# Optimization experiments

Hardware: AMD Instinct MI355X
Metric: run time of the kernel (lower is better)

The kernel has to match this reference:

```python
import jax, jax.numpy as jnp
import numpy as np

N_QUBITS = 4
DIM = 2 ** N_QUBITS  # 16-dim statevector
KERNEL = 3
STRIDE = 1
PADDING = 1


def _rot_mats(w):
    # PennyLane Rot(phi, theta, omega) = RZ(omega) RY(theta) RZ(phi)
    phi, theta, omega = w[:, 0], w[:, 1], w[:, 2]
    c = jnp.cos(theta / 2)
    s = jnp.sin(theta / 2)
    em = jnp.exp(-0.5j * (phi + omega))
    ep = jnp.exp(0.5j * (phi + omega))
    ed = jnp.exp(0.5j * (phi - omega))
    edm = jnp.exp(-0.5j * (phi - omega))
    row0 = jnp.stack([em * c, -ed * s], axis=-1)
    row1 = jnp.stack([edm * s, ep * c], axis=-1)
    return jnp.stack([row0, row1], axis=-2)  # [n_qubits, 2, 2]


def _apply_1q(state, U, wire):
    # state: [M] + [2]*n, wire axis is 1+wire (wire 0 is most significant)
    s = jnp.moveaxis(state, 1 + wire, -1)
    s = jnp.einsum('...b,ab->...a', s, U)
    return jnp.moveaxis(s, -1, 1 + wire)


def _apply_cnot(state, c, t):
    s = jnp.moveaxis(state, (1 + c, 1 + t), (-2, -1))
    shp = s.shape
    s = s.reshape(shp[:-2] + (4,))[..., jnp.array([0, 1, 3, 2])].reshape(shp)
    return jnp.moveaxis(s, (-2, -1), (1 + c, 1 + t))


def _forward(x, W_pre, b_pre, W_post, b_post, q_weights):
    B, C, L = x.shape
    xp = jnp.pad(x, ((0, 0), (0, 0), (PADDING, PADDING)))
    L_out = (L + 2 * PADDING - KERNEL) // STRIDE + 1
    starts = jnp.arange(L_out) * STRIDE
    # windows: [B, C, L_out, K] -> flatten channel-major like torch reshape
    win = xp[:, :, starts[:, None] + jnp.arange(KERNEL)[None, :]]
    win = win.transpose(0, 2, 1, 3).reshape(B, L_out, C * KERNEL)
    pre = win @ W_pre.T + b_pre  # [B, L_out, n_qubits]
    # AmplitudeEmbedding: pad to 2**n and normalize
    v = jnp.pad(pre, ((0, 0), (0, 0), (0, DIM - N_QUBITS)))
    v = v / jnp.linalg.norm(v, axis=-1, keepdims=True)
    state = v.reshape(B * L_out, *([2] * N_QUBITS)).astype(jnp.complex64)
    U = _rot_mats(q_weights)
    for i in range(N_QUBITS):
        state = _apply_1q(state, U[i], i)
    for i in range(N_QUBITS - 1):
        state = _apply_cnot(state, i, i + 1)
    flat = state.reshape(B * L_out, DIM)
    probs = jnp.real(flat) ** 2 + jnp.imag(flat) ** 2
    # PauliZ expectation per wire: sign of bit i (wire 0 = MSB)
    bits = (jnp.arange(DIM)[None, :] >> (N_QUBITS - 1 - jnp.arange(N_QUBITS)[:, None])) & 1
    z = (1 - 2 * bits).astype(probs.dtype)  # [n_qubits, DIM]
    expz = (probs @ z.T).reshape(B, L_out, N_QUBITS)
    out = expz @ W_post.T + b_post  # [B, L_out, out_channels]
    return out.transpose(0, 2, 1)


def setup_inputs() -> dict:
    key = jax.random.key(0)
    ks = jax.random.split(key, 6)
    B, C, L = 32, 80, 3000
    OUT = 512
    return {
        'x': jax.random.normal(ks[0], (B, C, L), dtype=jnp.float32),
        'W_pre': jax.random.normal(ks[1], (N_QUBITS, C * KERNEL), dtype=jnp.float32) * 0.06,
        'b_pre': jax.random.normal(ks[2], (N_QUBITS,), dtype=jnp.float32) * 0.06,
        'W_post': jax.random.normal(ks[3], (OUT, N_QUBITS), dtype=jnp.float32) * 0.4,
        'b_post': jax.random.normal(ks[4], (OUT,), dtype=jnp.float32) * 0.4,
        'q_weights': jax.random.normal(ks[5], (N_QUBITS, 3), dtype=jnp.float32),
    }


def reference(x, W_pre, b_pre, W_post, b_post, q_weights):
    return _forward(x, W_pre, b_pre, W_post, b_post, q_weights)
```

## Files before the change

### kernel.cpp

```cpp
#include <hip/hip_runtime.h>
#include <math.h>

#define C_IN 80
#define L_IN 3000
#define OUT_C 512
#define NT 256
#define TL 128

struct c2f { float x, y; };

__device__ __forceinline__ c2f cmul(c2f a, c2f b) {
    return { a.x*b.x - a.y*b.y, a.x*b.y + a.y*b.x };
}
__device__ __forceinline__ c2f csel(c2f a, c2f b, int bit) {
    c2f r; r.x = bit ? b.x : a.x; r.y = bit ? b.y : a.y; return r;
}
__device__ __forceinline__ float quadform(const float4* __restrict__ A, float4 p) {
    float4 r0 = A[0], r1 = A[1], r2 = A[2], r3 = A[3];
    return p.x*(r0.x*p.x + r0.y*p.y + r0.z*p.z + r0.w*p.w)
         + p.y*(r1.x*p.x + r1.y*p.y + r1.z*p.z + r1.w*p.w)
         + p.z*(r2.x*p.x + r2.y*p.y + r2.z*p.z + r2.w*p.w)
         + p.w*(r3.x*p.x + r3.y*p.y + r3.z*p.z + r3.w*p.w);
}

__global__ __launch_bounds__(NT) void qconv_kernel(
    const float* __restrict__ x,
    const float* __restrict__ W_pre,
    const float* __restrict__ b_pre,
    const float* __restrict__ W_post,
    const float* __restrict__ b_post,
    const float* __restrict__ qw,
    float* __restrict__ out)
{
    __shared__ float4 s_wpre[C_IN*3];
    __shared__ float4 s_post[OUT_C];
    __shared__ float  s_bpost[OUT_C];
    __shared__ float4 s_A[4][4];
    __shared__ float4 s_part[TL];
    __shared__ float4 s_e[TL];

    const int t  = threadIdx.x;
    const int b  = blockIdx.y;
    const int l0 = blockIdx.x * TL;

    for (int i = t; i < C_IN*3; i += NT) {
        s_wpre[i] = make_float4(W_pre[0*C_IN*3 + i], W_pre[1*C_IN*3 + i],
                                W_pre[2*C_IN*3 + i], W_pre[3*C_IN*3 + i]);
    }
    for (int i = t; i < OUT_C; i += NT) {
        s_post[i]  = *reinterpret_cast<const float4*>(&W_post[i*4]);
        s_bpost[i] = b_post[i];
    }
    __syncthreads();

    if (t < 64) {
        c2f U[4][2][2];
        #pragma unroll
        for (int i = 0; i < 4; ++i) {
            float phi = qw[i*3+0], theta = qw[i*3+1], omega = qw[i*3+2];
            float sh, ch;  sincosf(0.5f*theta, &sh, &ch);
            float s1, c1;  sincosf(0.5f*(phi+omega), &s1, &c1);
            float s2, cv;  sincosf(0.5f*(phi-omega), &s2, &cv);
            U[i][0][0] = {  c1*ch, -s1*ch };
            U[i][0][1] = { -cv*sh, -s2*sh };
            U[i][1][0] = {  cv*sh, -s2*sh };
            U[i][1][1] = {  c1*ch,  s1*ch };
        }
        const int q  = t >> 4;
        const int j  = (t >> 2) & 3;
        const int jp = t & 3;
        const int j2  = (j  >> 1) & 1, j3  = j  & 1;
        const int jp2 = (jp >> 1) & 1, jp3 = jp & 1;
        float s = 0.f;
        #pragma unroll
        for (int k = 0; k < 16; ++k) {
            int m = k ^ ((k >> 1) & 1);
            m ^= ((m >> 2) & 1) << 1;
            m ^= ((m >> 3) & 1) << 2;
            const int m0 = (m >> 3) & 1, m1 = (m >> 2) & 1;
            const int m2 = (m >> 1) & 1, m3 = m & 1;
            c2f w01 = cmul(U[0][m0][0], U[1][m1][0]);
            c2f av = cmul(w01, cmul(csel(U[2][m2][0], U[2][m2][1], j2),
                                    csel(U[3][m3][0], U[3][m3][1], j3)));
            c2f bv = cmul(w01, cmul(csel(U[2][m2][0], U[2][m2][1], jp2),
                                    csel(U[3][m3][0], U[3][m3][1], jp3)));
            float z = 1.f - 2.f * ((k >> (3 - q)) & 1);
            s += z * (av.x*bv.x + av.y*bv.y);
        }
        ((float*)s_A)[t] = s;
    }

    const int i = t & (TL - 1);
    const int h = t >> 7;
    const int l = l0 + i;
    const bool lvalid = (l < L_IN);

    float4 acc = (h == 0) ? make_float4(b_pre[0], b_pre[1], b_pre[2], b_pre[3])
                          : make_float4(0.f, 0.f, 0.f, 0.f);
    if (lvalid) {
        const float* __restrict__ xrow = x + (size_t)b * C_IN * L_IN + (size_t)(h*40) * L_IN + l;
        const bool has_m1 = (l >= 1);
        const bool has_p1 = (l + 1 < L_IN);
        #pragma unroll 4
        for (int c = 0; c < 40; ++c) {
            const float* r = xrow + c * L_IN;
            float xa = has_m1 ? r[-1] : 0.f;
            float xb = r[0];
            float xc = has_p1 ? r[1] : 0.f;
            float4 w0 = s_wpre[(h*40+c)*3+0], w1 = s_wpre[(h*40+c)*3+1], w2 = s_wpre[(h*40+c)*3+2];
            acc.x += w0.x*xa + w1.x*xb + w2.x*xc;
            acc.y += w0.y*xa + w1.y*xb + w2.y*xc;
            acc.z += w0.z*xa + w1.z*xb + w2.z*xc;
            acc.w += w0.w*xa + w1.w*xb + w2.w*xc;
        }
    }
    if (h == 1) s_part[i] = acc;
    __syncthreads();

    if (t < TL) {
        float4 p = acc;
        float4 q2 = s_part[t];
        p.x += q2.x; p.y += q2.y; p.z += q2.z; p.w += q2.w;
        const float inv = 1.f / (p.x*p.x + p.y*p.y + p.z*p.z + p.w*p.w);
        float4 e;
        e.x = quadform(s_A[0], p) * inv;
        e.y = quadform(s_A[1], p) * inv;
        e.z = quadform(s_A[2], p) * inv;
        e.w = quadform(s_A[3], p) * inv;
        s_e[t] = e;
    }
    __syncthreads();

    {
        const int lane = t & 63;
        const int w    = t >> 6;
        const int lc   = l0 + 2*lane;
        const bool v2  = (lc < L_IN);
        const float4 e0 = s_e[2*lane];
        const float4 e1 = s_e[2*lane + 1];
        float* op = out + (size_t)b * OUT_C * L_IN + (size_t)w * L_IN + lc;
        #pragma unroll 4
        for (int k = 0; k < OUT_C/4; ++k) {
            const int o = w + 4*k;
            float4 wv = s_post[o];
            float bb  = s_bpost[o];
            float2 st;
            st.x = wv.x*e0.x + wv.y*e0.y + wv.z*e0.z + wv.w*e0.w + bb;
            st.y = wv.x*e1.x + wv.y*e1.y + wv.z*e1.z + wv.w*e1.w + bb;
            if (v2) *reinterpret_cast<float2*>(op) = st;
            op += (size_t)4 * L_IN;
        }
    }
}

extern "C" void kernel_launch(void* const* d_in, const int* in_sizes, int n_in,
                              void* d_out, int out_size, void* d_ws, size_t ws_size,
                              hipStream_t stream) {
    const float* x      = (const float*)d_in[0];
    const float* W_pre  = (const float*)d_in[1];
    const float* b_pre  = (const float*)d_in[2];
    const float* W_post = (const float*)d_in[3];
    const float* b_post = (const float*)d_in[4];
    const float* qw     = (const float*)d_in[5];
    float* out = (float*)d_out;

    const int B = in_sizes[0] / (C_IN * L_IN);
    dim3 grid((L_IN + TL - 1) / TL, B);
    qconv_kernel<<<grid, NT, 0, stream>>>(x, W_pre, b_pre, W_post, b_post, qw, out);
}
```

Baseline: 46.97 us.

## Split into expz kernel and wide nontemporal-store expansion kernel

The fused kernel becomes two kernels. The first computes per-position PauliZ expectations and writes them to a workspace buffer. The second kernel uses 512 threads, reads those expectations and writes the 512-channel output as 16-byte nontemporal stores, four positions per thread. The aim is to make the output-write-bound stage store wider and with higher occupancy, separate from the input-reduction stage. The cost is an extra launch and a small workspace round trip.

Result: slower. 79.35 us (+68.9%).

```diff
diff --git a/kernel.cpp b/kernel.cpp
--- a/kernel.cpp
+++ b/kernel.cpp
@@ -4,8 +4,11 @@
 #define C_IN 80
 #define L_IN 3000
 #define OUT_C 512
-#define NT 256
 #define TL 128
+#define NT1 256
+#define NT2 512
+
+typedef float floatx4 __attribute__((ext_vector_type(4)));
 
 struct c2f { float x, y; };
 
@@ -23,33 +26,24 @@
          + p.w*(r3.x*p.x + r3.y*p.y + r3.z*p.z + r3.w*p.w);
 }
 
-__global__ __launch_bounds__(NT) void qconv_kernel(
+__global__ __launch_bounds__(NT1) void qconv_expz_kernel(
     const float* __restrict__ x,
     const float* __restrict__ W_pre,
     const float* __restrict__ b_pre,
-    const float* __restrict__ W_post,
-    const float* __restrict__ b_post,
     const float* __restrict__ qw,
-    float* __restrict__ out)
+    float4* __restrict__ expz)
 {
     __shared__ float4 s_wpre[C_IN*3];
-    __shared__ float4 s_post[OUT_C];
-    __shared__ float  s_bpost[OUT_C];
     __shared__ float4 s_A[4][4];
     __shared__ float4 s_part[TL];
-    __shared__ float4 s_e[TL];
 
     const int t  = threadIdx.x;
     const int b  = blockIdx.y;
     const int l0 = blockIdx.x * TL;
 
-    for (int i = t; i < C_IN*3; i += NT) {
+    for (int i = t; i < C_IN*3; i += NT1) {
         s_wpre[i] = make_float4(W_pre[0*C_IN*3 + i], W_pre[1*C_IN*3 + i],
                                 W_pre[2*C_IN*3 + i], W_pre[3*C_IN*3 + i]);
-    }
-    for (int i = t; i < OUT_C; i += NT) {
-        s_post[i]  = *reinterpret_cast<const float4*>(&W_post[i*4]);
-        s_bpost[i] = b_post[i];
     }
     __syncthreads();
 
@@ -117,7 +111,7 @@
     if (h == 1) s_part[i] = acc;
     __syncthreads();
 
-    if (t < TL) {
+    if (t < TL && lvalid) {
         float4 p = acc;
         float4 q2 = s_part[t];
         p.x += q2.x; p.y += q2.y; p.z += q2.z; p.w += q2.w;
@@ -127,29 +121,54 @@
         e.y = quadform(s_A[1], p) * inv;
         e.z = quadform(s_A[2], p) * inv;
         e.w = quadform(s_A[3], p) * inv;
-        s_e[t] = e;
+        expz[(size_t)b * L_IN + l] = e;
+    }
+}
+
+__global__ __launch_bounds__(NT2) void expand_kernel(
+    const float4* __restrict__ expz,
+    const float* __restrict__ W_post,
+    const float* __restrict__ b_post,
+    float* __restrict__ out)
+{
+    __shared__ float4 s_post[OUT_C];
+    __shared__ float  s_bpost[OUT_C];
+
+    const int t  = threadIdx.x;
+    const int b  = blockIdx.y;
+    const int l0 = blockIdx.x * TL;
+
+    s_post[t]  = *reinterpret_cast<const float4*>(&W_post[t*4]);
+    s_bpost[t] = b_post[t];
+
+    const int lane = t & 63;
+    const int w    = t >> 6;
+    const int lq   = lane & 31;
+    const int hi   = lane >> 5;
+    const int l    = l0 + 4*lq;
+    const bool v   = (l < L_IN);
+
+    float4 e0, e1, e2, e3;
+    if (v) {
+        const float4* ep = expz + (size_t)b * L_IN + l;
+        e0 = ep[0]; e1 = ep[1]; e2 = ep[2]; e3 = ep[3];
     }
     __syncthreads();
+    if (!v) return;
 
-    {
-        const int lane = t & 63;
-        const int w    = t >> 6;
-        const int lc   = l0 + 2*lane;
-        const bool v2  = (lc < L_IN);
-        const float4 e0 = s_e[2*lane];
-        const float4 e1 = s_e[2*lane + 1];
-        float* op = out + (size_t)b * OUT_C * L_IN + (size_t)w * L_IN + lc;
-        #pragma unroll 4
-        for (int k = 0; k < OUT_C/4; ++k) {
-            const int o = w + 4*k;
-            float4 wv = s_post[o];
-            float bb  = s_bpost[o];
-            float2 st;
-            st.x = wv.x*e0.x + wv.y*e0.y + wv.z*e0.z + wv.w*e0.w + bb;
-            st.y = wv.x*e1.x + wv.y*e1.y + wv.z*e1.z + wv.w*e1.w + bb;
-            if (v2) *reinterpret_cast<float2*>(op) = st;
-            op += (size_t)4 * L_IN;
-        }
+    float* op = out + (size_t)b * OUT_C * L_IN + (size_t)(w*2 + hi) * L_IN + l;
+    #pragma unroll 8
+    for (int k = 0; k < OUT_C/16; ++k) {
+        const int o = w*2 + hi + 16*k;
+        const float4 wv = s_post[o];
+        const float  bb = s_bpost[o];
+        floatx4 st;
+        st.x = wv.x*e0.x + wv.y*e0.y + wv.z*e0.z + wv.w*e0.w + bb;
+        st.y = wv.x*e1.x + wv.y*e1.y + wv.z*e1.z + wv.w*e1.w + bb;
+        st.z = wv.x*e2.x + wv.y*e2.y + wv.z*e2.z + wv.w*e2.w + bb;
+        st.w = wv.x*e3.x + wv.y*e3.y + wv.z*e3.z + wv.w*e3.w + bb;
+        __builtin_nontemporal_store(st, reinterpret_cast<floatx4*>(op));
+        op += (size_t)16 * L_IN;
     }
 }
 
@@ -163,8 +182,10 @@
     const float* b_post = (const float*)d_in[4];
     const float* qw     = (const float*)d_in[5];
     float* out = (float*)d_out;
+    float4* expz = (float4*)d_ws;
 
     const int B = in_sizes[0] / (C_IN * L_IN);
     dim3 grid((L_IN + TL - 1) / TL, B);
-    qconv_kernel<<<grid, NT, 0, stream>>>(x, W_pre, b_pre, W_post, b_post, qw, out);
+    qconv_expz_kernel<<<grid, NT1, 0, stream>>>(x, W_pre, b_pre, qw, expz);
+    expand_kernel<<<grid, NT2, 0, stream>>>(expz, W_post, b_post, out);
 }
```
